# Kernel optimization log

Hardware: AMD Instinct MI355X
Metric: run time of the kernel (lower is better)

The kernel has to match this reference:

```python
import jax, jax.numpy as jnp
import numpy as np

N = 100_000       # nodes
E = 1_600_000     # edges (avg degree 16)
IN_DIM = 256
OUT_DIM = 64
NEG_SLOPE = 0.01  # F.leaky_relu default


def setup_inputs() -> dict:
    key = jax.random.key(0)
    k1, k2, k3, k4, k5 = jax.random.split(key, 5)
    h = jax.random.normal(k1, (N, IN_DIM), jnp.float32)
    fc_w = jax.random.normal(k2, (IN_DIM, OUT_DIM), jnp.float32) / np.sqrt(IN_DIM)
    attn_w = jax.random.normal(k3, (2 * OUT_DIM,), jnp.float32) / np.sqrt(2 * OUT_DIM)
    src = jax.random.randint(k4, (E,), 0, N, jnp.int32)
    dst = jax.random.randint(k5, (E,), 0, N, jnp.int32)
    return {"h": h, "fc_w": fc_w, "attn_w": attn_w, "src": src, "dst": dst}


def reference(h, fc_w, attn_w, src, dst):
    # z = fc(h)
    z = h @ fc_w                                    # [N, D]
    # attn_fc(cat(z_src, z_dst)) == z_src @ a_l + z_dst @ a_r
    s_src = z @ attn_w[:OUT_DIM]                    # [N]
    s_dst = z @ attn_w[OUT_DIM:]                    # [N]
    e = jax.nn.leaky_relu(s_src[src] + s_dst[dst], NEG_SLOPE)  # [E]
    # per-destination segment softmax (stable)
    e_max = jax.ops.segment_max(e, dst, num_segments=N)        # [N]
    e_max = jnp.where(jnp.isfinite(e_max), e_max, 0.0)         # nodes w/o in-edges
    ex = jnp.exp(e - e_max[dst])                               # [E]
    denom = jax.ops.segment_sum(ex, dst, num_segments=N)       # [N]
    alpha = ex / jnp.maximum(denom[dst], 1e-9)                 # [E]
    # weighted scatter-sum of source features
    h_out = jax.ops.segment_sum(alpha[:, None] * z[src], dst, num_segments=N)  # [N, D]
    return h_out
```

## Files before the change

### kernel.cpp

```cpp
#include <hip/hip_runtime.h>
#include <hip/hip_bf16.h>
#include <math.h>

#define IN_DIM 256
#define OUT_DIM 64
#define NEG_SLOPE 0.01f
#define NBSHIFT 8
#define BCAP 5120
#define A_CHUNK 4096

typedef __attribute__((ext_vector_type(8))) short short8;
typedef __attribute__((ext_vector_type(4))) float f32x4;

__device__ __forceinline__ unsigned short f2bf_rne(float f) {
    unsigned u = __builtin_bit_cast(unsigned, f);
    u += 0x7FFF + ((u >> 16) & 1);
    return (unsigned short)(u >> 16);
}
__device__ __forceinline__ float bflo(unsigned v) {
    return __builtin_bit_cast(float, v << 16);
}
__device__ __forceinline__ float bfhi(unsigned v) {
    return __builtin_bit_cast(float, v & 0xFFFF0000u);
}
__device__ __forceinline__ unsigned cvtpk_bf16(float lo, float hi) {
    unsigned r;
    asm("v_cvt_pk_bf16_f32 %0, %1, %2" : "=v"(r) : "v"(lo), "v"(hi));
    return r;
}

__global__ __launch_bounds__(256) void k_prep(
    const float* __restrict__ fcw, unsigned short* __restrict__ bhi,
    int* __restrict__ gcnt, int NB)
{
    int t = blockIdx.x * 256 + threadIdx.x;
    if (t < NB) gcnt[t] = 0;
    if (t >= 2048) return;
    int lane = t & 63;
    int nt = (t >> 6) & 3;
    int step = t >> 8;
    int kbase = step * 32 + (lane >> 4) * 8;
    int col = nt * 16 + (lane & 15);
#pragma unroll
    for (int i = 0; i < 8; ++i)
        bhi[t * 8 + i] = f2bf_rne(fcw[(size_t)(kbase + i) * OUT_DIM + col]);
}

__global__ __launch_bounds__(256, 4) void k_gemm(
    const float* __restrict__ h, const unsigned short* __restrict__ bhi,
    const float* __restrict__ attnw, unsigned short* __restrict__ zb,
    float* __restrict__ ssrc, float* __restrict__ sdst, int nrows)
{
    __shared__ short8 Bs[2048];
    const int tid = threadIdx.x;
    const int lane = tid & 63;
    const int wid = tid >> 6;
    const int rowbase = blockIdx.x * 64 + wid * 16;
    const int arow = rowbase + (lane & 15);
    const size_t abase = (size_t)min(arow, nrows - 1) * IN_DIM + (lane >> 4) * 8;

    float4 a[16];
#pragma unroll
    for (int s = 0; s < 8; ++s) {
        a[2 * s]     = *(const float4*)&h[abase + s * 32];
        a[2 * s + 1] = *(const float4*)&h[abase + s * 32 + 4];
    }
    asm volatile("" ::: "memory");

    short8 breg[8];
#pragma unroll
    for (int c = 0; c < 8; ++c)
        breg[c] = *(const short8*)&bhi[(c * 256 + tid) * 8];
#pragma unroll
    for (int c = 0; c < 8; ++c)
        Bs[c * 256 + tid] = breg[c];
    __syncthreads();

    short8 abf[8];
#pragma unroll
    for (int step = 0; step < 8; ++step) {
        uint4 pk;
        pk.x = cvtpk_bf16(a[2 * step].x,     a[2 * step].y);
        pk.y = cvtpk_bf16(a[2 * step].z,     a[2 * step].w);
        pk.z = cvtpk_bf16(a[2 * step + 1].x, a[2 * step + 1].y);
        pk.w = cvtpk_bf16(a[2 * step + 1].z, a[2 * step + 1].w);
        abf[step] = __builtin_bit_cast(short8, pk);
    }

    f32x4 acc[4] = {};
#pragma unroll
    for (int step = 0; step < 8; ++step) {
#pragma unroll
        for (int nt = 0; nt < 4; ++nt) {
            short8 bh = Bs[(step * 4 + nt) * 64 + lane];
            acc[nt] = __builtin_amdgcn_mfma_f32_16x16x32_bf16(
                abf[step], bh, acc[nt], 0, 0, 0);
        }
    }

    const int col = lane & 15;
    float aw1[4], aw2[4];
#pragma unroll
    for (int nt = 0; nt < 4; ++nt) {
        aw1[nt] = attnw[nt * 16 + col];
        aw2[nt] = attnw[OUT_DIM + nt * 16 + col];
    }
#pragma unroll
    for (int r = 0; r < 4; ++r) {
        int grow = rowbase + (lane >> 4) * 4 + r;
        float ss = 0.f, sd = 0.f;
#pragma unroll
        for (int nt = 0; nt < 4; ++nt) {
            float v = acc[nt][r];
            ss = fmaf(v, aw1[nt], ss);
            sd = fmaf(v, aw2[nt], sd);
            if (grow < nrows)
                zb[(size_t)grow * OUT_DIM + nt * 16 + col] = f2bf_rne(v);
        }
#pragma unroll
        for (int m = 8; m; m >>= 1) {
            ss += __shfl_xor(ss, m);
            sd += __shfl_xor(sd, m);
        }
        if (col == 0 && grow < nrows) { ssrc[grow] = ss; sdst[grow] = sd; }
    }
}

__global__ __launch_bounds__(256) void k_bin(
    const int* __restrict__ src, const int* __restrict__ dst,
    int* __restrict__ gcnt, int* __restrict__ gbuf, int E, int NB)
{
    __shared__ int cnt[512];
    __shared__ int base[512];
    int t = threadIdx.x;
    for (int i = t; i < NB; i += 256) cnt[i] = 0;
    __syncthreads();
    int ebase = blockIdx.x * A_CHUNK;
    int bkt[16], pkd[16];
#pragma unroll
    for (int i = 0; i < 16; ++i) {
        int e = ebase + t + i * 256;
        bkt[i] = -1;
        if (e < E) {
            int d = dst[e];
            int b = ((unsigned)d) >> NBSHIFT;
            bkt[i] = b;
            pkd[i] = ((d & ((1 << NBSHIFT) - 1)) << 24) | src[e];
            atomicAdd(&cnt[b], 1);
        }
    }
    __syncthreads();
    for (int i = t; i < NB; i += 256) {
        int c = cnt[i];
        base[i] = c ? (i * BCAP + atomicAdd(&gcnt[i], c)) : 0;
    }
    __syncthreads();
#pragma unroll
    for (int i = 0; i < 16; ++i) {
        if (bkt[i] >= 0) {
            int r = atomicAdd(&base[bkt[i]], 1);
            gbuf[r] = pkd[i];
        }
    }
}

__global__ __launch_bounds__(256) void k_csr(
    const int* __restrict__ gcnt, const int* __restrict__ gbuf,
    const float* __restrict__ ssrc, const float* __restrict__ sdst,
    int2* __restrict__ rowse, int* __restrict__ csr_src,
    float* __restrict__ csr_w, int N)
{
    __shared__ int ldeg[256];
    __shared__ int cur[256];
    __shared__ float lsd[256];
    int t = threadIdx.x;
    int b = blockIdx.x;
    int eb = b * BCAP;
    int cnt = min(gcnt[b], BCAP);
    int node0 = (b << NBSHIFT) + t;
    ldeg[t] = 0;
    lsd[t] = (node0 < N) ? sdst[node0] : 0.f;
    __syncthreads();
    for (int i = t; i < cnt; i += 256)
        atomicAdd(&ldeg[((unsigned)gbuf[eb + i]) >> 24], 1);
    __syncthreads();
    int own = ldeg[t];
    for (int o = 1; o < 256; o <<= 1) {
        int x = 0;
        if (t >= o) x = ldeg[t - o];
        __syncthreads();
        if (t >= o) ldeg[t] += x;
        __syncthreads();
    }
    int excl = ldeg[t] - own;
    if (node0 < N) rowse[node0] = make_int2(eb + excl, eb + excl + own);
    cur[t] = excl;
    __syncthreads();

    for (int cb = 0; cb < cnt; cb += 4096) {
        const int nloc = min(4096, cnt - cb);
        int p[16]; float w[16];
#pragma unroll
        for (int k = 0; k < 16; ++k) {
            int i = t + k * 256;
            if (i < nloc) {
                p[k] = gbuf[eb + cb + i];
                float x = ssrc[p[k] & 0xFFFFFF] + lsd[((unsigned)p[k]) >> 24];
                x = (x > 0.f) ? x : NEG_SLOPE * x;
                w[k] = __expf(x);
            }
        }
#pragma unroll
        for (int k = 0; k < 16; ++k) {
            int i = t + k * 256;
            if (i < nloc) {
                int r = atomicAdd(&cur[((unsigned)p[k]) >> 24], 1);
                csr_src[eb + r] = p[k] & 0xFFFFFF;
                csr_w[eb + r] = w[k];
            }
        }
    }
}

__global__ __launch_bounds__(256) void k_node(
    const unsigned short* __restrict__ zb, const float* __restrict__ csr_w,
    const int2* __restrict__ rowse, const int* __restrict__ csr_src,
    float* __restrict__ out, int nnodes)
{
    __shared__ float lwo[16][130];
    const int t = threadIdx.x;
    const int g = t >> 4;
    const int li = t & 15;
    const int li8 = li * 8;
    const int node = blockIdx.x * 16 + g;
    int start = 0, end = 0;
    if (node < nnodes) { int2 se = rowse[node]; start = se.x; end = se.y; }

    float denom = 0.f;
    float acc0 = 0.f, acc1 = 0.f, acc2 = 0.f, acc3 = 0.f;

    for (int base = start; base < end; base += 64) {
        const int cnt = min(64, end - base);
        for (int i = li; i < cnt; i += 16) {
            lwo[g][2 * i]     = csr_w[base + i];
            lwo[g][2 * i + 1] = __builtin_bit_cast(float, csr_src[base + i] << 7);
        }
#pragma unroll 4
        for (int l = 0; l < cnt; ++l) {
            float2 pw = *(const float2*)&lwo[g][2 * l];
            const float w = pw.x;
            const int off = __builtin_bit_cast(int, pw.y) + li8;
            const uint2 v = *(const uint2*)((const char*)zb + off);
            acc0 = fmaf(w, bflo(v.x), acc0);
            acc1 = fmaf(w, bfhi(v.x), acc1);
            acc2 = fmaf(w, bflo(v.y), acc2);
            acc3 = fmaf(w, bfhi(v.y), acc3);
            denom += w;
        }
    }
    if (node < nnodes) {
        const float inv = 1.f / fmaxf(denom, 1e-9f);
        float4 o = make_float4(acc0 * inv, acc1 * inv, acc2 * inv, acc3 * inv);
        *(float4*)&out[(size_t)node * OUT_DIM + li * 4] = o;
    }
}

extern "C" void kernel_launch(void* const* d_in, const int* in_sizes, int n_in,
                              void* d_out, int out_size, void* d_ws, size_t ws_size,
                              hipStream_t stream)
{
    const float* h     = (const float*)d_in[0];
    const float* fcw   = (const float*)d_in[1];
    const float* attnw = (const float*)d_in[2];
    const int*   src   = (const int*)d_in[3];
    const int*   dst   = (const int*)d_in[4];
    const int N = in_sizes[0] / IN_DIM;
    const int E = in_sizes[3];
    float* out = (float*)d_out;

    const int NB = (N + 255) >> NBSHIFT;
    const int NWGA = (E + A_CHUNK - 1) / A_CHUNK;

    char* ws = (char*)d_ws;
    size_t off = 0;
    auto carve = [&](size_t bytes) -> void* {
        void* p = ws + off;
        off = (off + bytes + 255) & ~(size_t)255;
        return p;
    };
    unsigned short* zb = (unsigned short*)carve((size_t)N * OUT_DIM * 2);
    float* ssrc     = (float*)carve((size_t)N * 4);
    float* sdst     = (float*)carve((size_t)N * 4);
    int2*  rowse    = (int2*)carve((size_t)N * 8);
    int*   csr_src  = (int*)carve((size_t)NB * BCAP * 4);
    float* csr_w    = (float*)carve((size_t)NB * BCAP * 4);
    int*   gbuf     = (int*)carve((size_t)NB * BCAP * 4);
    unsigned short* bhi = (unsigned short*)carve(2048 * 8 * 2);
    int* gcnt  = (int*)carve((size_t)NB * 4);

    k_prep<<<8, 256, 0, stream>>>(fcw, bhi, gcnt, NB);
    k_gemm<<<(N + 63) / 64, 256, 0, stream>>>(h, bhi, attnw, zb, ssrc, sdst, N);
    k_bin<<<NWGA, 256, 0, stream>>>(src, dst, gcnt, gbuf, E, NB);
    k_csr<<<NB, 256, 0, stream>>>(gcnt, gbuf, ssrc, sdst, rowse, csr_src, csr_w, N);
    k_node<<<(N + 15) / 16, 256, 0, stream>>>(zb, csr_w, rowse, csr_src, out, N);
}
```

Baseline: 113.1 us.

## Stage GEMM A tile via global_load_lds and read B fragments directly from global

The GEMM kernel now loads the h rows straight into padded LDS with the global_load_lds direct-to-LDS path, one fully coalesced 1KB row per wave instruction, instead of strided per-lane float4 register loads. It then reads MFMA A fragments from LDS. The B (bf16 weight) tile is no longer staged in shared memory and is read from global/L2 per MFMA. The goal is better coalescing and fewer registers, but LDS use rises to about 66KB per block and occupancy drops to 2 blocks per CU, while B reads now go through cache on every step.

```diff
diff --git a/kernel.cpp b/kernel.cpp
--- a/kernel.cpp
+++ b/kernel.cpp
@@ -46,44 +46,44 @@
         bhi[t * 8 + i] = f2bf_rne(fcw[(size_t)(kbase + i) * OUT_DIM + col]);
 }
 
-__global__ __launch_bounds__(256, 4) void k_gemm(
+__global__ __launch_bounds__(256, 2) void k_gemm(
     const float* __restrict__ h, const unsigned short* __restrict__ bhi,
     const float* __restrict__ attnw, unsigned short* __restrict__ zb,
     float* __restrict__ ssrc, float* __restrict__ sdst, int nrows)
 {
-    __shared__ short8 Bs[2048];
+    __shared__ float As[64 * 260];
     const int tid = threadIdx.x;
     const int lane = tid & 63;
     const int wid = tid >> 6;
     const int rowbase = blockIdx.x * 64 + wid * 16;
-    const int arow = rowbase + (lane & 15);
-    const size_t abase = (size_t)min(arow, nrows - 1) * IN_DIM + (lane >> 4) * 8;
-
-    float4 a[16];
-#pragma unroll
-    for (int s = 0; s < 8; ++s) {
-        a[2 * s]     = *(const float4*)&h[abase + s * 32];
-        a[2 * s + 1] = *(const float4*)&h[abase + s * 32 + 4];
-    }
-    asm volatile("" ::: "memory");
-
-    short8 breg[8];
-#pragma unroll
-    for (int c = 0; c < 8; ++c)
-        breg[c] = *(const short8*)&bhi[(c * 256 + tid) * 8];
-#pragma unroll
-    for (int c = 0; c < 8; ++c)
-        Bs[c * 256 + tid] = breg[c];
-    __syncthreads();
-
+
+#pragma unroll
+    for (int rr = 0; rr < 16; ++rr) {
+        int grow = min(rowbase + rr, nrows - 1);
+        const float* gp = &h[(size_t)grow * IN_DIM + lane * 4];
+        float* lp = &As[(wid * 16 + rr) * 260];
+        __builtin_amdgcn_global_load_lds(
+            (const __attribute__((address_space(1))) void*)gp,
+            (__attribute__((address_space(3))) void*)lp, 16, 0, 0);
+    }
+    asm volatile("s_waitcnt vmcnt(0)" ::: "memory");
+    __builtin_amdgcn_sched_barrier(0);
+
+    const int Rbase = (wid * 16 + (lane & 15)) * 260 + (lane >> 4) * 8;
+    float4 af0[8], af1[8];
+#pragma unroll
+    for (int step = 0; step < 8; ++step) {
+        af0[step] = *(const float4*)&As[Rbase + step * 32];
+        af1[step] = *(const float4*)&As[Rbase + step * 32 + 4];
+    }
     short8 abf[8];
 #pragma unroll
     for (int step = 0; step < 8; ++step) {
         uint4 pk;
-        pk.x = cvtpk_bf16(a[2 * step].x,     a[2 * step].y);
-        pk.y = cvtpk_bf16(a[2 * step].z,     a[2 * step].w);
-        pk.z = cvtpk_bf16(a[2 * step + 1].x, a[2 * step + 1].y);
-        pk.w = cvtpk_bf16(a[2 * step + 1].z, a[2 * step + 1].w);
+        pk.x = cvtpk_bf16(af0[step].x, af0[step].y);
+        pk.y = cvtpk_bf16(af0[step].z, af0[step].w);
+        pk.z = cvtpk_bf16(af1[step].x, af1[step].y);
+        pk.w = cvtpk_bf16(af1[step].z, af1[step].w);
         abf[step] = __builtin_bit_cast(short8, pk);
     }
 
@@ -92,7 +92,7 @@
     for (int step = 0; step < 8; ++step) {
 #pragma unroll
         for (int nt = 0; nt < 4; ++nt) {
-            short8 bh = Bs[(step * 4 + nt) * 64 + lane];
+            short8 bh = *(const short8*)&bhi[((step * 4 + nt) * 64 + lane) * 8];
             acc[nt] = __builtin_amdgcn_mfma_f32_16x16x32_bf16(
                 abf[step], bh, acc[nt], 0, 0, 0);
         }
```

Result: slower. 118.1 us (+4.4%).

## Fuse CSR build and node aggregation into one per-bucket kernel with LDS pairs

Applied to the files above, without the earlier changes.

Merges the CSR construction and per-node aggregation kernels into a single kernel that builds each bucket's sorted (weight, offset) pairs in shared memory and aggregates directly from there. Buckets shrink from 256 to 128 destination nodes so the pair array fits in LDS. This removes the global write and reread of csr_src, csr_w and rowse plus one launch. In exchange each block now does serial per-node aggregation over 8 nodes per 16-lane group, which gives fewer blocks and less latency hiding, and the smaller per-bucket capacity raises the risk of overflow on skewed degrees.

```diff
diff --git a/kernel.cpp b/kernel.cpp
--- a/kernel.cpp
+++ b/kernel.cpp
@@ -5,8 +5,9 @@
 #define IN_DIM 256
 #define OUT_DIM 64
 #define NEG_SLOPE 0.01f
-#define NBSHIFT 8
-#define BCAP 5120
+#define NBSHIFT 7
+#define BNODES 128
+#define BCAP 2560
 #define A_CHUNK 4096
 
 typedef __attribute__((ext_vector_type(8))) short short8;
@@ -130,8 +131,8 @@
     const int* __restrict__ src, const int* __restrict__ dst,
     int* __restrict__ gcnt, int* __restrict__ gbuf, int E, int NB)
 {
-    __shared__ int cnt[512];
-    __shared__ int base[512];
+    __shared__ int cnt[1024];
+    __shared__ int base[1024];
     int t = threadIdx.x;
     for (int i = t; i < NB; i += 256) cnt[i] = 0;
     __syncthreads();
@@ -145,7 +146,7 @@
             int d = dst[e];
             int b = ((unsigned)d) >> NBSHIFT;
             bkt[i] = b;
-            pkd[i] = ((d & ((1 << NBSHIFT) - 1)) << 24) | src[e];
+            pkd[i] = ((d & (BNODES - 1)) << 24) | src[e];
             atomicAdd(&cnt[b], 1);
         }
     }
@@ -164,37 +165,43 @@
     }
 }
 
-__global__ __launch_bounds__(256) void k_csr(
+__global__ __launch_bounds__(256) void k_aggr(
     const int* __restrict__ gcnt, const int* __restrict__ gbuf,
     const float* __restrict__ ssrc, const float* __restrict__ sdst,
-    int2* __restrict__ rowse, int* __restrict__ csr_src,
-    float* __restrict__ csr_w, int N)
-{
-    __shared__ int ldeg[256];
-    __shared__ int cur[256];
-    __shared__ float lsd[256];
-    int t = threadIdx.x;
-    int b = blockIdx.x;
-    int eb = b * BCAP;
-    int cnt = min(gcnt[b], BCAP);
-    int node0 = (b << NBSHIFT) + t;
-    ldeg[t] = 0;
-    lsd[t] = (node0 < N) ? sdst[node0] : 0.f;
+    const unsigned short* __restrict__ zb, float* __restrict__ out, int N)
+{
+    __shared__ float2 pairs[BCAP];
+    __shared__ int   ldeg[BNODES];
+    __shared__ int   cur[BNODES];
+    __shared__ float lsd[BNODES];
+    __shared__ int2  se[BNODES];
+    const int t = threadIdx.x;
+    const int b = blockIdx.x;
+    const int eb = b * BCAP;
+    const int cnt = min(gcnt[b], BCAP);
+
+    if (t < BNODES) {
+        int node0 = (b << NBSHIFT) + t;
+        ldeg[t] = 0;
+        lsd[t] = (node0 < N) ? sdst[node0] : 0.f;
+    }
     __syncthreads();
     for (int i = t; i < cnt; i += 256)
         atomicAdd(&ldeg[((unsigned)gbuf[eb + i]) >> 24], 1);
     __syncthreads();
-    int own = ldeg[t];
-    for (int o = 1; o < 256; o <<= 1) {
+    int own = (t < BNODES) ? ldeg[t] : 0;
+    for (int o = 1; o < BNODES; o <<= 1) {
         int x = 0;
-        if (t >= o) x = ldeg[t - o];
+        if (t < BNODES && t >= o) x = ldeg[t - o];
         __syncthreads();
-        if (t >= o) ldeg[t] += x;
+        if (t < BNODES && t >= o) ldeg[t] += x;
         __syncthreads();
     }
-    int excl = ldeg[t] - own;
-    if (node0 < N) rowse[node0] = make_int2(eb + excl, eb + excl + own);
-    cur[t] = excl;
+    if (t < BNODES) {
+        int excl = ldeg[t] - own;
+        cur[t] = excl;
+        se[t] = make_int2(excl, excl + own);
+    }
     __syncthreads();
 
     for (int cb = 0; cb < cnt; cb += 4096) {
@@ -215,53 +222,37 @@
             int i = t + k * 256;
             if (i < nloc) {
                 int r = atomicAdd(&cur[((unsigned)p[k]) >> 24], 1);
-                csr_src[eb + r] = p[k] & 0xFFFFFF;
-                csr_w[eb + r] = w[k];
+                pairs[r] = make_float2(
+                    w[k], __builtin_bit_cast(float, (p[k] & 0xFFFFFF) << 7));
             }
         }
     }
-}
-
-__global__ __launch_bounds__(256) void k_node(
-    const unsigned short* __restrict__ zb, const float* __restrict__ csr_w,
-    const int2* __restrict__ rowse, const int* __restrict__ csr_src,
-    float* __restrict__ out, int nnodes)
-{
-    __shared__ float lwo[16][130];
-    const int t = threadIdx.x;
+    __syncthreads();
+
     const int g = t >> 4;
-    const int li = t & 15;
-    const int li8 = li * 8;
-    const int node = blockIdx.x * 16 + g;
-    int start = 0, end = 0;
-    if (node < nnodes) { int2 se = rowse[node]; start = se.x; end = se.y; }
-
-    float denom = 0.f;
-    float acc0 = 0.f, acc1 = 0.f, acc2 = 0.f, acc3 = 0.f;
-
-    for (int base = start; base < end; base += 64) {
-        const int cnt = min(64, end - base);
-        for (int i = li; i < cnt; i += 16) {
-            lwo[g][2 * i]     = csr_w[base + i];
-            lwo[g][2 * i + 1] = __builtin_bit_cast(float, csr_src[base + i] << 7);
-        }
+    const int li8 = (t & 15) * 8;
+#pragma unroll
+    for (int j = 0; j < BNODES / 16; ++j) {
+        const int ln = g * (BNODES / 16) + j;
+        const int node = (b << NBSHIFT) + ln;
+        if (node >= N) continue;
+        const int2 s = se[ln];
+        float denom = 0.f, a0 = 0.f, a1 = 0.f, a2 = 0.f, a3 = 0.f;
 #pragma unroll 4
-        for (int l = 0; l < cnt; ++l) {
-            float2 pw = *(const float2*)&lwo[g][2 * l];
+        for (int i = s.x; i < s.y; ++i) {
+            float2 pw = pairs[i];
             const float w = pw.x;
             const int off = __builtin_bit_cast(int, pw.y) + li8;
             const uint2 v = *(const uint2*)((const char*)zb + off);
-            acc0 = fmaf(w, bflo(v.x), acc0);
-            acc1 = fmaf(w, bfhi(v.x), acc1);
-            acc2 = fmaf(w, bflo(v.y), acc2);
-            acc3 = fmaf(w, bfhi(v.y), acc3);
+            a0 = fmaf(w, bflo(v.x), a0);
+            a1 = fmaf(w, bfhi(v.x), a1);
+            a2 = fmaf(w, bflo(v.y), a2);
+            a3 = fmaf(w, bfhi(v.y), a3);
             denom += w;
         }
-    }
-    if (node < nnodes) {
         const float inv = 1.f / fmaxf(denom, 1e-9f);
-        float4 o = make_float4(acc0 * inv, acc1 * inv, acc2 * inv, acc3 * inv);
-        *(float4*)&out[(size_t)node * OUT_DIM + li * 4] = o;
+        *(float4*)&out[(size_t)node * OUT_DIM + (t & 15) * 4] =
+            make_float4(a0 * inv, a1 * inv, a2 * inv, a3 * inv);
     }
 }
 
@@ -278,7 +269,7 @@
     const int E = in_sizes[3];
     float* out = (float*)d_out;
 
-    const int NB = (N + 255) >> NBSHIFT;
+    const int NB = (N + BNODES - 1) >> NBSHIFT;
     const int NWGA = (E + A_CHUNK - 1) / A_CHUNK;
 
     char* ws = (char*)d_ws;
@@ -291,9 +282,6 @@
     unsigned short* zb = (unsigned short*)carve((size_t)N * OUT_DIM * 2);
     float* ssrc     = (float*)carve((size_t)N * 4);
     float* sdst     = (float*)carve((size_t)N * 4);
-    int2*  rowse    = (int2*)carve((size_t)N * 8);
-    int*   csr_src  = (int*)carve((size_t)NB * BCAP * 4);
-    float* csr_w    = (float*)carve((size_t)NB * BCAP * 4);
     int*   gbuf     = (int*)carve((size_t)NB * BCAP * 4);
     unsigned short* bhi = (unsigned short*)carve(2048 * 8 * 2);
     int* gcnt  = (int*)carve((size_t)NB * 4);
@@ -301,6 +289,5 @@
     k_prep<<<8, 256, 0, stream>>>(fcw, bhi, gcnt, NB);
     k_gemm<<<(N + 63) / 64, 256, 0, stream>>>(h, bhi, attnw, zb, ssrc, sdst, N);
     k_bin<<<NWGA, 256, 0, stream>>>(src, dst, gcnt, gbuf, E, NB);
-    k_csr<<<NB, 256, 0, stream>>>(gcnt, gbuf, ssrc, sdst, rowse, csr_src, csr_w, N);
-    k_node<<<(N + 15) / 16, 256, 0, stream>>>(zb, csr_w, rowse, csr_src, out, N);
-}
+    k_aggr<<<NB, 256, 0, stream>>>(gcnt, gbuf, ssrc, sdst, zb, out, N);
+}
```

New measurement: 102.0 us. -9.8%, faster.
